# Optimization experiments

Hardware: AMD Instinct MI355X
Metric: run time of the kernel (lower is better)

The kernel has to match this reference:

```python
import math
import jax, jax.numpy as jnp
import numpy as np

B, T, D, H = 2, 2048, 1024, 16
N_LAYERS = 24


def get_slopes(n):
    def pow2(n):
        start = 2 ** (-2 ** (-(math.log2(n) - 3)))
        return [start * start ** i for i in range(n)]
    if math.log2(n).is_integer():
        return pow2(n)
    c = 2 ** math.floor(math.log2(n))
    return pow2(c) + get_slopes(2 * c)[0::2][: n - c]


def setup_inputs() -> dict:
    key = jax.random.key(0)
    ks = jax.random.split(key, 5)
    x = jax.random.normal(ks[0], (B, T, D), dtype=jnp.float32)
    Wq = 0.02 * jax.random.normal(ks[1], (D, D), dtype=jnp.float32)
    Wk = 0.02 * jax.random.normal(ks[2], (D, D), dtype=jnp.float32)
    Wv = 0.02 * jax.random.normal(ks[3], (D, D), dtype=jnp.float32)
    Wo = (0.02 / math.sqrt(2 * N_LAYERS)) * jax.random.normal(ks[4], (D, D), dtype=jnp.float32)
    z = jnp.zeros((D,), dtype=jnp.float32)
    return {"x": x, "Wq": Wq, "bq": z, "Wk": Wk, "bk": z, "Wv": Wv, "bv": z, "Wo": Wo, "bo": z}


def reference(x, Wq, bq, Wk, bk, Wv, bv, Wo, bo):
    Bb, Tt, C = x.shape
    hd = C // H
    # QKV projections -> (B, H, T, hd)
    q = (x @ Wq + bq).reshape(Bb, Tt, H, hd).transpose(0, 2, 1, 3)
    k = (x @ Wk + bk).reshape(Bb, Tt, H, hd).transpose(0, 2, 1, 3)
    v = (x @ Wv + bv).reshape(Bb, Tt, H, hd).transpose(0, 2, 1, 3)
    # scaled dot-product scores (B, H, T, T)
    attn = jnp.einsum('bhqd,bhkd->bhqk', q, k) / jnp.sqrt(jnp.asarray(hd, x.dtype))
    # ALiBi bias: module uses only last row of the relative-position matrix,
    # broadcast over query positions: -slope_h * (T-1 - j), shape (1, H, 1, T)
    slopes = jnp.asarray(get_slopes(H), dtype=x.dtype)
    alibi = -slopes[None, :, None, None] * (Tt - 1 - jnp.arange(Tt, dtype=x.dtype))[None, None, None, :]
    attn = attn + alibi
    # causal mask
    causal = jnp.tril(jnp.ones((Tt, Tt), dtype=bool))[None, None, :, :]
    attn = jnp.where(causal, attn, jnp.finfo(x.dtype).min)
    p = jax.nn.softmax(attn, axis=-1)
    out = jnp.einsum('bhqk,bhkd->bqhd', p, v).reshape(Bb, Tt, C)
    return out @ Wo + bo
```

## Files before the change

kernel.cpp:

```cpp
#include <hip/hip_runtime.h>
#include <hip/hip_bf16.h>

#define Bn 2
#define Tdim 2048
#define Ddim 1024
#define Hn 16
#define HD 64

typedef unsigned short u16;
typedef unsigned int u32;
typedef __attribute__((ext_vector_type(8))) __bf16 bf16x8;
typedef __attribute__((ext_vector_type(4))) float f32x4;
typedef __attribute__((ext_vector_type(16))) float f32x16;
typedef __attribute__((ext_vector_type(4))) u32 u32x4;

struct alignas(8) U16x4 { u16 x, y, z, w; };

__device__ __forceinline__ u16 f2bf(float f) {
  union { float f; u32 i; } v; v.f = f;
  u32 x = v.i;
  u32 r = (x + 0x7fffu + ((x >> 16) & 1u)) >> 16;
  return (u16)r;
}
__device__ __forceinline__ float bf2f(u16 u) {
  union { u32 i; float f; } v; v.i = ((u32)u) << 16; return v.f;
}

__device__ __forceinline__ u32 cvtpk_bf16(float a, float b) {
  u32 d;
  asm("v_cvt_pk_bf16_f32 %0, %1, %2" : "=v"(d) : "v"(a), "v"(b));
  return d;
}

__device__ __forceinline__ void cp16(const u16* g, u16* l) {
  __builtin_amdgcn_global_load_lds(
      (const __attribute__((address_space(1))) u32*)g,
      (__attribute__((address_space(3))) u32*)l, 16, 0, 0);
}

__device__ __forceinline__ f32x4 mfma16(bf16x8 a, bf16x8 b, f32x4 c) {
  return __builtin_amdgcn_mfma_f32_16x16x32_bf16(a, b, c, 0, 0, 0);
}
__device__ __forceinline__ f32x16 mfma32(bf16x8 a, bf16x8 b, f32x16 c) {
  return __builtin_amdgcn_mfma_f32_32x32x16_bf16(a, b, c, 0, 0, 0);
}

__global__ __launch_bounds__(256) void preproc_k(
    const float* __restrict__ x, u16* __restrict__ Xb,
    const float* __restrict__ s0, const float* __restrict__ s1,
    const float* __restrict__ s2, const float* __restrict__ s3,
    u16* __restrict__ dstW) {
  const int tx = threadIdx.x, ty = threadIdx.y;
  if (blockIdx.z == 4) {
    const int tid = ty * 32 + tx;
    const int i = ((blockIdx.y * 32 + blockIdx.x) * 256 + tid) * 16;
#pragma unroll
    for (int c = 0; c < 2; c++) {
      u16 t[8];
#pragma unroll
      for (int j = 0; j < 8; j++) t[j] = f2bf(x[i + c * 8 + j]);
      *(bf16x8*)&Xb[i + c * 8] = *(const bf16x8*)t;
    }
    return;
  }
  const float* src = (blockIdx.z == 0) ? s0 : (blockIdx.z == 1) ? s1
                   : (blockIdx.z == 2) ? s2 : s3;
  u16* d = dstW + (size_t)blockIdx.z * Ddim * Ddim;
  __shared__ u16 tile[32][33];
  const int xx = blockIdx.x * 32 + tx;
  const int y0 = blockIdx.y * 32;
#pragma unroll
  for (int j = 0; j < 32; j += 8) tile[ty + j][tx] = f2bf(src[(size_t)(y0 + ty + j) * Ddim + xx]);
  __syncthreads();
  const int xo = blockIdx.y * 32 + tx;
  const int yo0 = blockIdx.x * 32;
#pragma unroll
  for (int j = 0; j < 32; j += 8) d[(size_t)(yo0 + ty + j) * Ddim + xo] = tile[tx][ty + j];
}

__global__ __launch_bounds__(256, 2) void gemm_qkv(
    const u16* __restrict__ Xb, const u16* __restrict__ WT,
    const float* __restrict__ bq, const float* __restrict__ bk, const float* __restrict__ bv,
    u16* __restrict__ Q, u16* __restrict__ K, u16* __restrict__ Vt) {
  const int flat = blockIdx.x + 32 * (blockIdx.y + 8 * blockIdx.z);
  const int l = (flat & 7) * 96 + (flat >> 3);
  const int lbx = l & 31, lby = (l >> 5) & 7, z = l >> 8;

  const u16* Wt = WT + (size_t)z * Ddim * Ddim;
  const float* bias = (z == 0) ? bq : (z == 1) ? bk : bv;
  u16* QK = (z == 0) ? Q : K;

  __shared__ alignas(16) u16 Alds[128 * 64];
  __shared__ alignas(16) u16 Blds[128 * 64];
  const int tid = threadIdx.x;
  const int w = tid >> 6, lane = tid & 63, ln = lane & 15, quad = lane >> 4;
  const int wm = (w >> 1) * 64, wn = (w & 1) * 64;
  const int tm = lbx * 128, tn = lby * 128;

  f32x4 acc[4][4] = {};

  const int srow = lane >> 3;
  const int scol = ((lane & 7) ^ srow) * 8;
  const u16* ag0 = Xb + (size_t)(tm + w * 32 + srow) * Ddim + scol;
  const u16* bg0 = Wt + (size_t)(tn + w * 32 + srow) * Ddim + scol;

#define QKV_KLOOP(MFMA_EXPR)                                                  \
  for (int k0 = 0; k0 < Ddim; k0 += 64) {                                     \
    __syncthreads();                                                          \
    _Pragma("unroll")                                                         \
    for (int j = 0; j < 4; j++) {                                             \
      cp16(ag0 + (size_t)j * 8 * Ddim + k0, &Alds[(w * 32 + j * 8) * 64]);    \
      cp16(bg0 + (size_t)j * 8 * Ddim + k0, &Blds[(w * 32 + j * 8) * 64]);    \
    }                                                                         \
    __syncthreads();                                                          \
    _Pragma("unroll")                                                         \
    for (int k2 = 0; k2 < 2; k2++) {                                          \
      const int so = ((k2 * 4 + quad) ^ (ln & 7)) * 8;                        \
      bf16x8 af[4], bfr[4];                                                   \
      _Pragma("unroll")                                                       \
      for (int i = 0; i < 4; i++)                                             \
        af[i] = *(const bf16x8*)&Alds[(wm + i * 16 + ln) * 64 + so];          \
      _Pragma("unroll")                                                       \
      for (int i = 0; i < 4; i++)                                             \
        bfr[i] = *(const bf16x8*)&Blds[(wn + i * 16 + ln) * 64 + so];         \
      _Pragma("unroll")                                                       \
      for (int mi = 0; mi < 4; mi++)                                          \
        _Pragma("unroll")                                                     \
        for (int ni = 0; ni < 4; ni++)                                        \
          acc[mi][ni] = MFMA_EXPR;                                            \
    }                                                                         \
  }

  if (z < 2) {
    QKV_KLOOP(mfma16(bfr[ni], af[mi], acc[mi][ni]))
    float bv4[4][4];
#pragma unroll
    for (int ni = 0; ni < 4; ni++)
#pragma unroll
      for (int r = 0; r < 4; r++)
        bv4[ni][r] = bias[tn + wn + ni * 16 + quad * 4 + r];
#pragma unroll
    for (int mi = 0; mi < 4; mi++) {
      const int gm = tm + wm + mi * 16 + ln;
      const int b0 = gm >> 11, t0 = gm & 2047;
#pragma unroll
      for (int ni = 0; ni < 4; ni++) {
        const int gnq = tn + wn + ni * 16 + quad * 4;
        const int hh = gnq >> 6, dd = gnq & 63;
        U16x4 pk;
        pk.x = f2bf(acc[mi][ni][0] + bv4[ni][0]);
        pk.y = f2bf(acc[mi][ni][1] + bv4[ni][1]);
        pk.z = f2bf(acc[mi][ni][2] + bv4[ni][2]);
        pk.w = f2bf(acc[mi][ni][3] + bv4[ni][3]);
        *(U16x4*)&QK[((size_t)(b0 * Hn + hh) * Tdim + t0) * HD + dd] = pk;
      }
    }
  } else {
    QKV_KLOOP(mfma16(af[mi], bfr[ni], acc[mi][ni]))
#pragma unroll
    for (int mi = 0; mi < 4; mi++) {
#pragma unroll
      for (int ni = 0; ni < 4; ni++) {
        const int gm0 = tm + wm + mi * 16 + quad * 4;
        const int gn = tn + wn + ni * 16 + ln;
        const float bv_ = bias[gn];
        const int hh = gn >> 6, dd = gn & 63;
        const int b0 = gm0 >> 11, t0 = gm0 & 2047;
        U16x4 pk;
        pk.x = f2bf(acc[mi][ni][0] + bv_);
        pk.y = f2bf(acc[mi][ni][1] + bv_);
        pk.z = f2bf(acc[mi][ni][2] + bv_);
        pk.w = f2bf(acc[mi][ni][3] + bv_);
        *(U16x4*)&Vt[((size_t)(b0 * Hn + hh) * HD + dd) * Tdim + t0] = pk;
      }
    }
  }
#undef QKV_KLOOP
}

#define KSTR 68
#define VSTR 132
#define L2E 1.44269504088896f
__global__ __launch_bounds__(256, 2) void attn_k(
    const u16* __restrict__ Q, const u16* __restrict__ K, const u16* __restrict__ Vt,
    u16* __restrict__ Op, float* __restrict__ lp) {
  __shared__ alignas(16) u16 Klds[2][128 * KSTR];
  __shared__ alignas(16) u16 Vtlds[2][64 * VSTR];

  const int id = blockIdx.x;
  const int xcd = id & 7, slot = id >> 3;
  const int bh = (xcd << 2) | (slot >> 4);
  const int inner = slot & 15;
  const int p = inner >> 1;
  const int s = inner & 1;
  const int tid = threadIdx.x;
  const int w = tid >> 6, lane = tid & 63;
  const int qi = lane & 31, hf = lane >> 5;

  const u16* Qh = Q + (size_t)bh * Tdim * HD;
  const u16* Kh = K + (size_t)bh * Tdim * HD;
  const u16* Vh = Vt + (size_t)bh * HD * Tdim;
  const float slope = exp2f(-0.5f * (float)((bh & 15) + 1));

  const float sl2 = slope * L2E;
  const float c1 = 0.125f * L2E;
  const float f4hf = (float)(4 * hf);
  float sg8[4], slm[4];
#pragma unroll
  for (int g = 0; g < 4; g++) sg8[g] = sl2 * (float)(8 * g);
#pragma unroll
  for (int m = 0; m < 4; m++) slm[m] = sl2 * (float)m;

  const int qbs[2] = {p, 15 - p};
  int K0[2], K1[2];
#pragma unroll
  for (int seg = 0; seg < 2; seg++) {
    const int nk = qbs[seg] + 1;
    const int h0 = (nk + 1) >> 1;
    K0[seg] = s ? h0 : 0;
    K1[seg] = s ? nk : h0;
  }

  bf16x8 kreg[4], vreg[4];
  {
    const int kb = ((K0[0] < K1[0]) ? K0[0] : K0[1]) * 128;
#pragma unroll
    for (int c = 0; c < 4; c++) {
      const int e = c * 2048 + tid * 8;
      kreg[c] = *(const bf16x8*)&Kh[(size_t)(kb + (e >> 6)) * HD + (e & 63)];
      vreg[c] = *(const bf16x8*)&Vh[(size_t)(e >> 7) * Tdim + kb + (e & 127)];
    }
#pragma unroll
    for (int c = 0; c < 4; c++) {
      const int e = c * 2048 + tid * 8;
      *(bf16x8*)&Klds[0][(e >> 6) * KSTR + (e & 63)] = kreg[c];
      *(bf16x8*)&Vtlds[0][(e >> 7) * VSTR + (e & 127)] = vreg[c];
    }
  }
  int cb = 0;

  for (int seg = 0; seg < 2; seg++) {
    const int qb = qbs[seg];
    const int kt0 = K0[seg], kt1 = K1[seg];
    const int nkt = qb + 1;
    const int q0 = qb * 128;
    const int tg = q0 + w * 32 + qi;
    const float tt2 = (slope * (float)tg + 3.0f) * L2E;

    bf16x8 qf[4];
#pragma unroll
    for (int kc = 0; kc < 4; kc++)
      qf[kc] = *(const bf16x8*)&Qh[(size_t)tg * HD + kc * 16 + hf * 8];

    float ls0 = 0.f, ls1 = 0.f;
    f32x16 oacc[2] = {};

    for (int kt = kt0; kt < kt1; kt++) {
      const int kb = kt * 128;
      __syncthreads();

      const int nxt = (kt + 1 < kt1) ? (kt + 1) : ((seg == 0) ? K0[1] : -1);
      if (nxt >= 0) {
        const int kb2 = nxt * 128;
#pragma unroll
        for (int c = 0; c < 4; c++) {
          const int e = c * 2048 + tid * 8;
          kreg[c] = *(const bf16x8*)&Kh[(size_t)(kb2 + (e >> 6)) * HD + (e & 63)];
          vreg[c] = *(const bf16x8*)&Vh[(size_t)(e >> 7) * Tdim + kb2 + (e & 127)];
        }
      }

      f32x16 st[4] = {};
      __builtin_amdgcn_s_setprio(1);
#pragma unroll
      for (int kc = 0; kc < 4; kc++) {
#pragma unroll
        for (int ni = 0; ni < 4; ni++) {
          bf16x8 kf = *(const bf16x8*)&Klds[cb][(ni * 32 + qi) * KSTR + kc * 16 + hf * 8];
          st[ni] = mfma32(kf, qf[kc], st[ni]);
        }
      }
      __builtin_amdgcn_s_setprio(0);

      const bool diag = (kt == nkt - 1);
      const float fkb = (float)kb + f4hf;
      bf16x8 pfrag[8];
#pragma unroll
      for (int ni = 0; ni < 4; ni++) {
        const float cni = __builtin_fmaf(sl2, fkb + (float)(32 * ni), -tt2);
        float pv[16];
        if (!diag) {
#pragma unroll
          for (int ri = 0; ri < 16; ri++) {
            const float e = __builtin_fmaf(st[ni][ri], c1, cni + sg8[ri >> 2] + slm[ri & 3]);
            const float pp = __builtin_amdgcn_exp2f(e);
            if (ri & 1) ls1 += pp; else ls0 += pp;
            pv[ri] = pp;
          }
        } else {
#pragma unroll
          for (int ri = 0; ri < 16; ri++) {
            const int n = kb + ni * 32 + (ri & 3) + 8 * (ri >> 2) + 4 * hf;
            const float e = __builtin_fmaf(st[ni][ri], c1, cni + sg8[ri >> 2] + slm[ri & 3]);
            float pp = __builtin_amdgcn_exp2f(e);
            if (n > tg) pp = 0.f;
            if (ri & 1) ls1 += pp; else ls0 += pp;
            pv[ri] = pp;
          }
        }
        u32 pk[4][2];
#pragma unroll
        for (int g = 0; g < 4; g++) {
          pk[g][0] = cvtpk_bf16(pv[g * 4 + 0], pv[g * 4 + 1]);
          pk[g][1] = cvtpk_bf16(pv[g * 4 + 2], pv[g * 4 + 3]);
        }
#pragma unroll
        for (int a = 0; a < 2; a++) {
          const u32 snd0 = (hf == 0) ? pk[2 * a + 1][0] : pk[2 * a][0];
          const u32 snd1 = (hf == 0) ? pk[2 * a + 1][1] : pk[2 * a][1];
          const u32 rcv0 = (u32)__shfl_xor((int)snd0, 32);
          const u32 rcv1 = (u32)__shfl_xor((int)snd1, 32);
          u32x4 fr;
          fr.x = (hf == 0) ? pk[2 * a][0] : rcv0;
          fr.y = (hf == 0) ? pk[2 * a][1] : rcv1;
          fr.z = (hf == 0) ? rcv0 : pk[2 * a + 1][0];
          fr.w = (hf == 0) ? rcv1 : pk[2 * a + 1][1];
          pfrag[ni * 2 + a] = *(bf16x8*)&fr;
        }
      }

      if (nxt >= 0) {
#pragma unroll
        for (int c = 0; c < 4; c++) {
          const int e = c * 2048 + tid * 8;
          *(bf16x8*)&Klds[cb ^ 1][(e >> 6) * KSTR + (e & 63)] = kreg[c];
          *(bf16x8*)&Vtlds[cb ^ 1][(e >> 7) * VSTR + (e & 127)] = vreg[c];
        }
      }

      __builtin_amdgcn_s_setprio(1);
#pragma unroll
      for (int kf16 = 0; kf16 < 8; kf16++) {
#pragma unroll
        for (int nd = 0; nd < 2; nd++) {
          bf16x8 vf = *(const bf16x8*)&Vtlds[cb][(nd * 32 + qi) * VSTR + kf16 * 16 + hf * 8];
          oacc[nd] = mfma32(pfrag[kf16], vf, oacc[nd]);
        }
      }
      __builtin_amdgcn_s_setprio(0);

      cb ^= 1;
    }

    float lsum = ls0 + ls1;
    lsum += __shfl_xor(lsum, 32);
    if (hf == 0) lp[(size_t)s * 65536 + bh * Tdim + tg] = lsum;

    u16* Ob = Op + (size_t)s * (32u * Tdim * HD) + ((size_t)bh * Tdim) * HD;
#pragma unroll
    for (int nd = 0; nd < 2; nd++) {
#pragma unroll
      for (int ri = 0; ri < 16; ri++) {
        const int rq = (ri & 3) + 8 * (ri >> 2) + 4 * hf;
        const int t = q0 + w * 32 + rq;
        Ob[(size_t)t * HD + nd * 32 + qi] = f2bf(oacc[nd][ri]);
      }
    }
  }
}

__global__ __launch_bounds__(256, 2) void gemm_out(
    const u16* __restrict__ Op, const float* __restrict__ lp,
    const u16* __restrict__ WoT, const float* __restrict__ bo,
    float* __restrict__ C) {
  const int flat = blockIdx.x + 64 * blockIdx.y;
  const int c = flat & 7, j = flat >> 3;
  const int lbx = c * 8 + (j & 7);
  const int lby = j >> 3;

  __shared__ alignas(16) u16 Alds[64 * 64];
  __shared__ alignas(16) u16 Blds[128 * 64];
  const int tid = threadIdx.x;
  const int w = tid >> 6, lane = tid & 63, ln = lane & 15, quad = lane >> 4;
  const int tm = lbx * 64, tn = lby * 128;

  f32x4 acc[4][2] = {};

  const int srow = lane >> 3;
  const int scol = ((lane & 7) ^ srow) * 8;
  const u16* bg0 = WoT + (size_t)(tn + w * 32 + srow) * Ddim + scol;

  const int ar = tid >> 3;
  const int ac8 = tid & 7;
  const int row0 = tm + ar, row1 = tm + ar + 32;
  const int b0r = row0 >> 11, t0r = row0 & 2047;
  const int b1r = row1 >> 11, t1r = row1 & 2047;
  const size_t pstr = (size_t)32 * Tdim * HD;
  const int aslot = (ac8 ^ (ar & 7)) * 8;

  u32x4 a00, a01, a10, a11;
  float l0a, l0b, l1a, l1b;
#define LOADA(H)                                                              \
  {                                                                           \
    const int bh0 = b0r * Hn + (H), bh1 = b1r * Hn + (H);                     \
    const size_t o0 = ((size_t)bh0 * Tdim + t0r) * HD + ac8 * 8;              \
    const size_t o1 = ((size_t)bh1 * Tdim + t1r) * HD + ac8 * 8;              \
    a00 = *(const u32x4*)&Op[o0];                                             \
    a01 = *(const u32x4*)&Op[pstr + o0];                                      \
    a10 = *(const u32x4*)&Op[o1];                                             \
    a11 = *(const u32x4*)&Op[pstr + o1];                                      \
    l0a = lp[bh0 * Tdim + t0r]; l0b = lp[65536 + bh0 * Tdim + t0r];           \
    l1a = lp[bh1 * Tdim + t1r]; l1b = lp[65536 + bh1 * Tdim + t1r];           \
  }

  LOADA(0);

  for (int k0 = 0; k0 < Ddim; k0 += 64) {
    __syncthreads();
#pragma unroll
    for (int jj = 0; jj < 4; jj++)
      cp16(bg0 + (size_t)jj * 8 * Ddim + k0, &Blds[(w * 32 + jj * 8) * 64]);
    {
      const float inv0 = 1.0f / (l0a + l0b);
      const float inv1 = 1.0f / (l1a + l1b);
      u32x4 q0, q1;
#pragma unroll
      for (int jj = 0; jj < 4; jj++) {
        const float lo0 = bf2f((u16)(a00[jj] & 0xffffu)) + bf2f((u16)(a01[jj] & 0xffffu));
        const float hi0 = bf2f((u16)(a00[jj] >> 16)) + bf2f((u16)(a01[jj] >> 16));
        q0[jj] = cvtpk_bf16(lo0 * inv0, hi0 * inv0);
        const float lo1 = bf2f((u16)(a10[jj] & 0xffffu)) + bf2f((u16)(a11[jj] & 0xffffu));
        const float hi1 = bf2f((u16)(a10[jj] >> 16)) + bf2f((u16)(a11[jj] >> 16));
        q1[jj] = cvtpk_bf16(lo1 * inv1, hi1 * inv1);
      }
      *(u32x4*)&Alds[ar * 64 + aslot] = q0;
      *(u32x4*)&Alds[(ar + 32) * 64 + aslot] = q1;
    }
    __syncthreads();
    if (k0 + 64 < Ddim) LOADA((k0 >> 6) + 1);
#pragma unroll
    for (int k2 = 0; k2 < 2; k2++) {
      const int so = ((k2 * 4 + quad) ^ (ln & 7)) * 8;
      bf16x8 af[4], bfr[2];
#pragma unroll
      for (int i = 0; i < 4; i++)
        af[i] = *(const bf16x8*)&Alds[(i * 16 + ln) * 64 + so];
#pragma unroll
      for (int i = 0; i < 2; i++)
        bfr[i] = *(const bf16x8*)&Blds[(w * 32 + i * 16 + ln) * 64 + so];
#pragma unroll
      for (int mi = 0; mi < 4; mi++)
#pragma unroll
        for (int ni = 0; ni < 2; ni++)
          acc[mi][ni] = mfma16(af[mi], bfr[ni], acc[mi][ni]);
    }
  }
#undef LOADA

#pragma unroll
  for (int mi = 0; mi < 4; mi++) {
#pragma unroll
    for (int ni = 0; ni < 2; ni++) {
      const int gm0 = tm + mi * 16 + quad * 4;
      const int gn = tn + w * 32 + ni * 16 + ln;
      const float bv_ = bo[gn];
#pragma unroll
      for (int r = 0; r < 4; r++)
        C[(size_t)(gm0 + r) * Ddim + gn] = acc[mi][ni][r] + bv_;
    }
  }
}

extern "C" void kernel_launch(void* const* d_in, const int* in_sizes, int n_in,
                              void* d_out, int out_size, void* d_ws, size_t ws_size,
                              hipStream_t stream) {
  (void)in_sizes; (void)n_in; (void)out_size; (void)ws_size;
  const float* x  = (const float*)d_in[0];
  const float* Wq = (const float*)d_in[1];
  const float* bq = (const float*)d_in[2];
  const float* Wk = (const float*)d_in[3];
  const float* bk = (const float*)d_in[4];
  const float* Wv = (const float*)d_in[5];
  const float* bv = (const float*)d_in[6];
  const float* Wo = (const float*)d_in[7];
  const float* bo = (const float*)d_in[8];

  char* ws = (char*)d_ws;
  const size_t MB = 1024 * 1024;
  u16* WT   = (u16*)(ws + 0 * MB);
  u16* Qb   = (u16*)(ws + 8 * MB);
  u16* Kb   = (u16*)(ws + 16 * MB);
  u16* Vtb  = (u16*)(ws + 24 * MB);
  u16* Xb   = (u16*)(ws + 32 * MB);
  u16* Opart= (u16*)(ws + 40 * MB);
  float* lpart = (float*)(ws + 56 * MB);
  u16* WoT = WT + (size_t)3 * Ddim * Ddim;

  preproc_k<<<dim3(32, 32, 5), dim3(32, 8), 0, stream>>>(x, Xb, Wq, Wk, Wv, Wo, WT);
  gemm_qkv<<<dim3(32, 8, 3), 256, 0, stream>>>(Xb, WT, bq, bk, bv, Qb, Kb, Vtb);
  attn_k<<<dim3(512), 256, 0, stream>>>(Qb, Kb, Vtb, Opart, lpart);
  gemm_out<<<dim3(64, 8), 256, 0, stream>>>(Opart, lpart, WoT, bo, (float*)d_out);
}
```

Measured before the change: 181.2 us.

## Single-buffer attention K/V LDS tiles and vectorize weight transpose stores

The attention kernel moves from double-buffered K/V shared-memory tiles to a single buffer. The register-prefetched tile is stored at the top of each iteration between two barriers, then the next tile's global loads are issued. This halves LDS use per block, which may allow more resident blocks, but adds a second barrier per iteration and shrinks the overlap between the LDS write and compute. Separately, the weight-transpose preprocessing now writes two bf16 values per 32-bit store instead of one u16 per store.

Result: no change. 180.3 us (-0.5%).

```diff
diff --git a/kernel.cpp b/kernel.cpp
--- a/kernel.cpp
+++ b/kernel.cpp
@@ -51,8 +51,8 @@
     const float* __restrict__ s2, const float* __restrict__ s3,
     u16* __restrict__ dstW) {
   const int tx = threadIdx.x, ty = threadIdx.y;
+  const int tid = ty * 32 + tx;
   if (blockIdx.z == 4) {
-    const int tid = ty * 32 + tx;
     const int i = ((blockIdx.y * 32 + blockIdx.x) * 256 + tid) * 16;
 #pragma unroll
     for (int c = 0; c < 2; c++) {
@@ -72,10 +72,16 @@
 #pragma unroll
   for (int j = 0; j < 32; j += 8) tile[ty + j][tx] = f2bf(src[(size_t)(y0 + ty + j) * Ddim + xx]);
   __syncthreads();
-  const int xo = blockIdx.y * 32 + tx;
+  const int c2 = (tid & 15) * 2;
+  const int rr = tid >> 4;
   const int yo0 = blockIdx.x * 32;
-#pragma unroll
-  for (int j = 0; j < 32; j += 8) d[(size_t)(yo0 + ty + j) * Ddim + xo] = tile[tx][ty + j];
+  const int xo0 = blockIdx.y * 32;
+#pragma unroll
+  for (int j = 0; j < 2; j++) {
+    const int r = rr + 16 * j;
+    const u32 vlo = tile[c2][r], vhi = tile[c2 + 1][r];
+    *(u32*)&d[(size_t)(yo0 + r) * Ddim + xo0 + c2] = vlo | (vhi << 16);
+  }
 }
 
 __global__ __launch_bounds__(256, 2) void gemm_qkv(
@@ -184,8 +190,8 @@
 __global__ __launch_bounds__(256, 2) void attn_k(
     const u16* __restrict__ Q, const u16* __restrict__ K, const u16* __restrict__ Vt,
     u16* __restrict__ Op, float* __restrict__ lp) {
-  __shared__ alignas(16) u16 Klds[2][128 * KSTR];
-  __shared__ alignas(16) u16 Vtlds[2][64 * VSTR];
+  __shared__ alignas(16) u16 Klds[128 * KSTR];
+  __shared__ alignas(16) u16 Vtlds[64 * VSTR];
 
   const int id = blockIdx.x;
   const int xcd = id & 7, slot = id >> 3;
@@ -230,14 +236,7 @@
       kreg[c] = *(const bf16x8*)&Kh[(size_t)(kb + (e >> 6)) * HD + (e & 63)];
       vreg[c] = *(const bf16x8*)&Vh[(size_t)(e >> 7) * Tdim + kb + (e & 127)];
     }
-#pragma unroll
-    for (int c = 0; c < 4; c++) {
-      const int e = c * 2048 + tid * 8;
-      *(bf16x8*)&Klds[0][(e >> 6) * KSTR + (e & 63)] = kreg[c];
-      *(bf16x8*)&Vtlds[0][(e >> 7) * VSTR + (e & 127)] = vreg[c];
-    }
-  }
-  int cb = 0;
+  }
 
   for (int seg = 0; seg < 2; seg++) {
     const int qb = qbs[seg];
@@ -258,15 +257,24 @@
     for (int kt = kt0; kt < kt1; kt++) {
       const int kb = kt * 128;
       __syncthreads();
-
-      const int nxt = (kt + 1 < kt1) ? (kt + 1) : ((seg == 0) ? K0[1] : -1);
-      if (nxt >= 0) {
-        const int kb2 = nxt * 128;
-#pragma unroll
-        for (int c = 0; c < 4; c++) {
-          const int e = c * 2048 + tid * 8;
-          kreg[c] = *(const bf16x8*)&Kh[(size_t)(kb2 + (e >> 6)) * HD + (e & 63)];
-          vreg[c] = *(const bf16x8*)&Vh[(size_t)(e >> 7) * Tdim + kb2 + (e & 127)];
+#pragma unroll
+      for (int c = 0; c < 4; c++) {
+        const int e = c * 2048 + tid * 8;
+        *(bf16x8*)&Klds[(e >> 6) * KSTR + (e & 63)] = kreg[c];
+        *(bf16x8*)&Vtlds[(e >> 7) * VSTR + (e & 127)] = vreg[c];
+      }
+      __syncthreads();
+
+      {
+        const int nxt = (kt + 1 < kt1) ? (kt + 1) : ((seg == 0) ? K0[1] : -1);
+        if (nxt >= 0) {
+          const int kb2 = nxt * 128;
+#pragma unroll
+          for (int c = 0; c < 4; c++) {
+            const int e = c * 2048 + tid * 8;
+            kreg[c] = *(const bf16x8*)&Kh[(size_t)(kb2 + (e >> 6)) * HD + (e & 63)];
+            vreg[c] = *(const bf16x8*)&Vh[(size_t)(e >> 7) * Tdim + kb2 + (e & 127)];
+          }
         }
       }
 
@@ -276,7 +284,7 @@
       for (int kc = 0; kc < 4; kc++) {
 #pragma unroll
         for (int ni = 0; ni < 4; ni++) {
-          bf16x8 kf = *(const bf16x8*)&Klds[cb][(ni * 32 + qi) * KSTR + kc * 16 + hf * 8];
+          bf16x8 kf = *(const bf16x8*)&Klds[(ni * 32 + qi) * KSTR + kc * 16 + hf * 8];
           st[ni] = mfma32(kf, qf[kc], st[ni]);
         }
       }
@@ -329,27 +337,16 @@
         }
       }
 
-      if (nxt >= 0) {
-#pragma unroll
-        for (int c = 0; c < 4; c++) {
-          const int e = c * 2048 + tid * 8;
-          *(bf16x8*)&Klds[cb ^ 1][(e >> 6) * KSTR + (e & 63)] = kreg[c];
-          *(bf16x8*)&Vtlds[cb ^ 1][(e >> 7) * VSTR + (e & 127)] = vreg[c];
-        }
-      }
-
       __builtin_amdgcn_s_setprio(1);
 #pragma unroll
       for (int kf16 = 0; kf16 < 8; kf16++) {
 #pragma unroll
         for (int nd = 0; nd < 2; nd++) {
-          bf16x8 vf = *(const bf16x8*)&Vtlds[cb][(nd * 32 + qi) * VSTR + kf16 * 16 + hf * 8];
+          bf16x8 vf = *(const bf16x8*)&Vtlds[(nd * 32 + qi) * VSTR + kf16 * 16 + hf * 8];
           oacc[nd] = mfma32(pfrag[kf16], vf, oacc[nd]);
         }
       }
       __builtin_amdgcn_s_setprio(0);
-
-      cb ^= 1;
     }
 
     float lsum = ls0 + ls1;
```
